# Kernel optimization log

Hardware: AMD Instinct MI355X
Metric: run time of the kernel (lower is better)

## Reference

```python
import jax, jax.numpy as jnp
import numpy as np

MARGIN = 0.2
BETA = 0.8333333
EPS = 1e-8          # torch cosine_similarity eps
BIG = 1.0e9         # sentinel used by the torch code for masking

B, M, FEAT, RES = 64, 2048, 512, 32


def setup_inputs() -> dict:
    key = jax.random.key(0)
    k1, k2, k3, k4 = jax.random.split(key, 4)
    return {
        "anchor_features": jax.random.normal(k1, (B, FEAT), dtype=jnp.float32),
        "true_voxels": jax.random.uniform(k2, (B, RES, RES, RES), dtype=jnp.float32),
        "memory_keys": jax.random.normal(k3, (M, FEAT), dtype=jnp.float32),
        "memory_values": jax.random.uniform(k4, (M, RES, RES, RES), dtype=jnp.float32),
    }


def reference(anchor_features, true_voxels, memory_keys, memory_values):
    b = true_voxels.shape[0]
    m = memory_values.shape[0]
    v = true_voxels.reshape(b, -1)        # (B, N) with N = res^3
    w = memory_values.reshape(m, -1)      # (M, N)
    n = v.shape[1]

    # Pairwise voxel MSE via ||a||^2 - 2ab + ||b||^2 GEMM trick (same math,
    # avoids the (B, M, N) broadcast intermediate).
    v_sq = jnp.sum(v * v, axis=1)                         # (B,)
    w_sq = jnp.sum(w * w, axis=1)                         # (M,)
    mse = (v_sq[:, None] + w_sq[None, :] - 2.0 * (v @ w.T)) / n   # (B, M)
    sv_scores = 1.0 - mse

    pos_mask = sv_scores > BETA
    neg_mask = sv_scores < BETA

    # Pairwise cosine distance 1 - cos_sim (norms clamped at eps like torch).
    a_norm = jnp.maximum(jnp.linalg.norm(anchor_features, axis=1, keepdims=True), EPS)
    k_norm = jnp.maximum(jnp.linalg.norm(memory_keys, axis=1, keepdims=True), EPS)
    key_dists = 1.0 - (anchor_features / a_norm) @ (memory_keys / k_norm).T  # (B, M)

    hardest_pos = jnp.max(jnp.where(pos_mask, key_dists, -BIG), axis=1)  # (B,)
    hardest_neg = jnp.min(jnp.where(neg_mask, key_dists, BIG), axis=1)   # (B,)

    loss = jnp.maximum(hardest_pos - hardest_neg + MARGIN, 0.0)          # (B,)

    valid = jnp.any(pos_mask, axis=1) & jnp.any(neg_mask, axis=1)        # (B,)
    cnt = jnp.sum(valid.astype(loss.dtype))
    total = jnp.sum(jnp.where(valid, loss, 0.0))
    # Masked mean; 0.0 when no valid triplets (mirrors the torch early-return).
    return jnp.where(cnt > 0, total / jnp.maximum(cnt, 1.0), 0.0)
```

## Files before the change

### kernel.cpp

```cpp
#include <hip/hip_runtime.h>


typedef __attribute__((ext_vector_type(8)))  short bf16x8;
typedef __attribute__((ext_vector_type(16))) float f32x16;

constexpr int   Mdim   = 2048;
constexpr int   Nvox   = 32768;
constexpr int   NS     = 32;
constexpr float BETA   = 0.8333333f;
constexpr float MARGIN = 0.2f;
constexpr float BIGV   = 1.0e9f;

constexpr size_t OFF_VSQ  = 0;
constexpr size_t OFF_AINV = 64;
constexpr size_t OFF_KINV = 128;
constexpr size_t OFF_WSQ  = 2176;
constexpr size_t OFF_WSQP = 4224;
constexpr size_t OFF_PHP  = 69760;
constexpr size_t OFF_PHN  = 70016;
constexpr size_t OFF_PAP  = 70272;
constexpr size_t OFF_PAN  = 70528;
constexpr size_t OFF_KEYP = 70784;
constexpr size_t OFF_DOTP = 201856;
constexpr size_t OFF_VHI  = 4396160;
constexpr size_t OFF_VLO  = 5444736;

__device__ __forceinline__ unsigned int bf16rne(float x) {
    unsigned int u = __float_as_uint(x);
    return (u + 0x7FFFu + ((u >> 16) & 1u)) >> 16;
}
__device__ __forceinline__ int pk2(unsigned int lo, unsigned int hi) {
    return (int)(lo | (hi << 16));
}
__device__ __forceinline__ void async16(const ushort* g, ushort* l) {
    __builtin_amdgcn_global_load_lds(
        (const __attribute__((address_space(1))) unsigned int*)g,
        (__attribute__((address_space(3))) unsigned int*)l, 16, 0, 0);
}

__global__ __launch_bounds__(256) void prep_kernel(
    const float* __restrict__ vox, const float* __restrict__ anc,
    const float* __restrict__ keys,
    ushort* __restrict__ vhi, ushort* __restrict__ vlo,
    float* __restrict__ vsq, float* __restrict__ ainv, float* __restrict__ kinv)
{
    const int tid = threadIdx.x;
    const int lane = tid & 63;
    const int wave = tid >> 6;
    if (blockIdx.x < 512) {
        #pragma unroll
        for (int u = 0; u < 2; ++u) {
            const int uid = blockIdx.x * 8 + wave * 2 + u;
            const int bh = uid & 1, s = (uid >> 1) & 3, c = uid >> 3;
            const int b   = bh * 32 + (lane & 31);
            const int col = c * 64 + s * 16 + (lane >> 5) * 8;
            const float4* src = reinterpret_cast<const float4*>(vox + (size_t)b * Nvox + col);
            const float4 x0 = src[0], x1 = src[1];
            const float e[8] = {x0.x, x0.y, x0.z, x0.w, x1.x, x1.y, x1.z, x1.w};
            unsigned int h[8], l8[8];
            #pragma unroll
            for (int q = 0; q < 8; ++q) {
                const unsigned int hb = bf16rne(e[q]);
                h[q] = hb;
                l8[q] = bf16rne(e[q] - __uint_as_float(hb << 16));
            }
            const int4 hp = { pk2(h[0],h[1]), pk2(h[2],h[3]), pk2(h[4],h[5]), pk2(h[6],h[7]) };
            const int4 lp = { pk2(l8[0],l8[1]), pk2(l8[2],l8[3]), pk2(l8[4],l8[5]), pk2(l8[6],l8[7]) };
            const size_t base = (size_t)c * 4096 + bh * 2048 + s * 512 + lane * 8;
            *reinterpret_cast<int4*>(vhi + base) = hp;
            *reinterpret_cast<int4*>(vlo + base) = lp;
        }
    } else if (blockIdx.x < 576) {
        const int b = blockIdx.x - 512;
        const float4* src = reinterpret_cast<const float4*>(vox + (size_t)b * Nvox);
        float p = 0.f;
        for (int i = tid; i < Nvox / 4; i += 256) {
            const float4 x = src[i];
            p = fmaf(x.x, x.x, p); p = fmaf(x.y, x.y, p);
            p = fmaf(x.z, x.z, p); p = fmaf(x.w, x.w, p);
        }
        #pragma unroll
        for (int off = 32; off > 0; off >>= 1) p += __shfl_down(p, off);
        __shared__ float sb[4];
        if (lane == 0) sb[wave] = p;
        __syncthreads();
        if (tid == 0) vsq[b] = sb[0] + sb[1] + sb[2] + sb[3];
    } else {
        const int r = (blockIdx.x - 576) * 4 + wave;
        const float* src = (r < 64) ? (anc + (size_t)r * 512)
                                    : (keys + (size_t)(r - 64) * 512);
        const float4* s4 = reinterpret_cast<const float4*>(src);
        const float4 x = s4[lane];
        const float4 y = s4[lane + 64];
        float p = 0.f;
        p = fmaf(x.x, x.x, p); p = fmaf(x.y, x.y, p);
        p = fmaf(x.z, x.z, p); p = fmaf(x.w, x.w, p);
        p = fmaf(y.x, y.x, p); p = fmaf(y.y, y.y, p);
        p = fmaf(y.z, y.z, p); p = fmaf(y.w, y.w, p);
        #pragma unroll
        for (int off = 32; off > 0; off >>= 1) p += __shfl_down(p, off);
        if (lane == 0) {
            const float inv = 1.f / fmaxf(sqrtf(p), 1e-8f);
            if (r < 64) ainv[r] = inv; else kinv[r - 64] = inv;
        }
    }
}

__global__ __launch_bounds__(256, 4) void gemm_big(
    const ushort* __restrict__ vhi, const ushort* __restrict__ vlo,
    const float* __restrict__ W,
    float* __restrict__ dotp, float* __restrict__ wsqp)
{
    __shared__ ushort sVhi[4096], sVlo[4096], sW[4096];
    __shared__ float red[256];

    const int tid  = threadIdx.x;
    const int lane = tid & 63;
    const int wave = tid >> 6;
    const int mb   = blockIdx.x & 31;
    const int ns   = blockIdx.x >> 5;
    const int srow = tid >> 2;
    const int sq   = tid & 3;

    const float*  wptr = W + (size_t)(mb * 64 + srow) * Nvox + ns * 1024 + sq * 4;
    const ushort* vhig = vhi + (size_t)(ns * 16) * 4096 + wave * 1024 + lane * 8;
    const ushort* vlog = vlo + (size_t)(ns * 16) * 4096 + wave * 1024 + lane * 8;
    ushort* ldsVhi = &sVhi[wave * 1024];
    ushort* ldsVlo = &sVlo[wave * 1024];

    const int wr = wave >> 1, wc = wave & 1;
    f32x16 acc = {};
    float wsq = 0.f;

    float4 wreg[4];
    #pragma unroll
    for (int j = 0; j < 4; ++j) wreg[j] = *reinterpret_cast<const float4*>(wptr + j * 16);

    const int woffbase = (srow >> 5) * 2048 + ((srow & 31) + 32 * (sq >> 1)) * 8 + (sq & 1) * 4;

    for (int ch = 0; ch < 16; ++ch) {
        int2 pj[4];
        #pragma unroll
        for (int j = 0; j < 4; ++j) {
            const float e[4] = {wreg[j].x, wreg[j].y, wreg[j].z, wreg[j].w};
            unsigned int hb[4];
            #pragma unroll
            for (int q = 0; q < 4; ++q) {
                wsq = fmaf(e[q], e[q], wsq);
                hb[q] = bf16rne(e[q]);
            }
            pj[j] = (int2){ pk2(hb[0], hb[1]), pk2(hb[2], hb[3]) };
        }
        __syncthreads();
        async16(vhig + (size_t)ch * 4096,       ldsVhi);
        async16(vhig + (size_t)ch * 4096 + 512, ldsVhi + 512);
        async16(vlog + (size_t)ch * 4096,       ldsVlo);
        async16(vlog + (size_t)ch * 4096 + 512, ldsVlo + 512);
        #pragma unroll
        for (int j = 0; j < 4; ++j)
            *reinterpret_cast<int2*>(&sW[woffbase + j * 512]) = pj[j];
        if (ch < 15) {
            #pragma unroll
            for (int j = 0; j < 4; ++j)
                wreg[j] = *reinterpret_cast<const float4*>(wptr + (ch + 1) * 64 + j * 16);
        }
        __syncthreads();
        #pragma unroll
        for (int s = 0; s < 4; ++s) {
            const bf16x8 ah = *reinterpret_cast<const bf16x8*>(&sVhi[wr * 2048 + s * 512 + lane * 8]);
            const bf16x8 al = *reinterpret_cast<const bf16x8*>(&sVlo[wr * 2048 + s * 512 + lane * 8]);
            const bf16x8 bh = *reinterpret_cast<const bf16x8*>(&sW[wc * 2048 + s * 512 + lane * 8]);
            acc = __builtin_amdgcn_mfma_f32_32x32x16_bf16(ah, bh, acc, 0, 0, 0);
            acc = __builtin_amdgcn_mfma_f32_32x32x16_bf16(al, bh, acc, 0, 0, 0);
        }
    }

    const int col   = lane & 31;
    const int rbase = 4 * (lane >> 5);
    const size_t out_m = (size_t)(mb * 64 + wc * 32 + col);
    #pragma unroll
    for (int r = 0; r < 16; ++r) {
        const int row = (r & 3) + 8 * (r >> 2) + rbase;
        const int b   = wr * 32 + row;
        dotp[(size_t)(ns * 64 + b) * Mdim + out_m] = acc[r];
    }
    red[tid] = wsq;
    __syncthreads();
    if (tid < 64)
        wsqp[(size_t)ns * Mdim + mb * 64 + tid] =
            red[tid*4] + red[tid*4+1] + red[tid*4+2] + red[tid*4+3];
}

__global__ __launch_bounds__(256) void keydist_kernel(
    const float* __restrict__ anc, const float* __restrict__ keys,
    const float* __restrict__ wsqp, float* __restrict__ keyp,
    float* __restrict__ wsq)
{
    const int tid = threadIdx.x;
    if (blockIdx.x >= 256) {
        const int m = (blockIdx.x - 256) * 256 + tid;
        float s = 0.f;
        #pragma unroll
        for (int sp = 0; sp < NS; ++sp) s += wsqp[(size_t)sp * Mdim + m];
        wsq[m] = s;
        return;
    }
    __shared__ float kk[8 * 516];
    const int mt = blockIdx.x * 8;
    {
        const int row = tid >> 5, colb = (tid & 31) * 16;
        const float4* src = reinterpret_cast<const float4*>(keys + (size_t)(mt + row) * 512 + colb);
        #pragma unroll
        for (int j = 0; j < 4; ++j)
            *reinterpret_cast<float4*>(&kk[row * 516 + colb + j * 4]) = src[j];
    }
    __syncthreads();
    const int b = tid >> 2, msub = tid & 3;
    const float* arow = anc + (size_t)b * 512;
    const float* k0 = &kk[msub * 516];
    const float* k1 = &kk[(msub + 4) * 516];
    float d0 = 0.f, d1 = 0.f;
    for (int k = 0; k < 512; k += 4) {
        const float4 a = *reinterpret_cast<const float4*>(arow + k);
        const float4 x = *reinterpret_cast<const float4*>(k0 + k);
        const float4 y = *reinterpret_cast<const float4*>(k1 + k);
        d0 = fmaf(a.x, x.x, d0); d0 = fmaf(a.y, x.y, d0);
        d0 = fmaf(a.z, x.z, d0); d0 = fmaf(a.w, x.w, d0);
        d1 = fmaf(a.x, y.x, d1); d1 = fmaf(a.y, y.y, d1);
        d1 = fmaf(a.z, y.z, d1); d1 = fmaf(a.w, y.w, d1);
    }
    keyp[(size_t)b * Mdim + mt + msub]     = d0;
    keyp[(size_t)b * Mdim + mt + msub + 4] = d1;
}

__global__ __launch_bounds__(256) void rowpart_kernel(
    const float* __restrict__ dotp, const float* __restrict__ wsq,
    const float* __restrict__ keyp, const float* __restrict__ vsq,
    const float* __restrict__ ainv, const float* __restrict__ kinv,
    float* __restrict__ php, float* __restrict__ phn,
    float* __restrict__ pap, float* __restrict__ pan)
{
    const int bid = blockIdx.x, tid = threadIdx.x;
    const int b = bid >> 2, sl = bid & 3;
    const float vs = vsq[b];
    const float ai = ainv[b];
    float hp = -BIGV, hn = BIGV, ap = 0.f, an = 0.f;
    #pragma unroll
    for (int rep = 0; rep < 2; ++rep) {
        const int m = sl * 512 + rep * 256 + tid;
        float dot = 0.f;
        #pragma unroll
        for (int s = 0; s < NS; ++s) dot += dotp[(size_t)(s * 64 + b) * Mdim + m];
        const float sv = 1.f - (vs + wsq[m] - 2.f * dot) * (1.f / 32768.f);
        const float kd = 1.f - keyp[(size_t)b * Mdim + m] * ai * kinv[m];
        if (sv > BETA) { ap = 1.f; hp = fmaxf(hp, kd); }
        if (sv < BETA) { an = 1.f; hn = fminf(hn, kd); }
    }
    #pragma unroll
    for (int off = 32; off > 0; off >>= 1) {
        hp = fmaxf(hp, __shfl_down(hp, off));
        hn = fminf(hn, __shfl_down(hn, off));
        ap = fmaxf(ap, __shfl_down(ap, off));
        an = fmaxf(an, __shfl_down(an, off));
    }
    __shared__ float sb[16];
    const int wv = tid >> 6;
    if ((tid & 63) == 0) {
        sb[wv * 4 + 0] = hp; sb[wv * 4 + 1] = hn;
        sb[wv * 4 + 2] = ap; sb[wv * 4 + 3] = an;
    }
    __syncthreads();
    if (tid == 0) {
        for (int w2 = 1; w2 < 4; ++w2) {
            hp = fmaxf(hp, sb[w2 * 4 + 0]);
            hn = fminf(hn, sb[w2 * 4 + 1]);
            ap = fmaxf(ap, sb[w2 * 4 + 2]);
            an = fmaxf(an, sb[w2 * 4 + 3]);
        }
        php[bid] = hp; phn[bid] = hn; pap[bid] = ap; pan[bid] = an;
    }
}

__global__ void final_kernel(const float* __restrict__ php, const float* __restrict__ phn,
                             const float* __restrict__ pap, const float* __restrict__ pan,
                             float* __restrict__ out)
{
    const int t = threadIdx.x;
    float hp = php[t], hn = phn[t], ap = pap[t], an = pan[t];
    hp = fmaxf(hp, __shfl_down(hp, 2)); hp = fmaxf(hp, __shfl_down(hp, 1));
    hn = fminf(hn, __shfl_down(hn, 2)); hn = fminf(hn, __shfl_down(hn, 1));
    ap = fmaxf(ap, __shfl_down(ap, 2)); ap = fmaxf(ap, __shfl_down(ap, 1));
    an = fmaxf(an, __shfl_down(an, 2)); an = fmaxf(an, __shfl_down(an, 1));
    __shared__ float sl[64], sc[64];
    if ((t & 3) == 0) {
        const int b = t >> 2;
        const float valid = (ap > 0.f && an > 0.f) ? 1.f : 0.f;
        sl[b] = fmaxf(hp - hn + MARGIN, 0.f) * valid;
        sc[b] = valid;
    }
    __syncthreads();
    if (t < 64) {
        float l = sl[t], c = sc[t];
        #pragma unroll
        for (int off = 32; off > 0; off >>= 1) {
            l += __shfl_down(l, off);
            c += __shfl_down(c, off);
        }
        if (t == 0) out[0] = (c > 0.f) ? (l / c) : 0.f;
    }
}

extern "C" void kernel_launch(void* const* d_in, const int* in_sizes, int n_in,
                              void* d_out, int out_size, void* d_ws, size_t ws_size,
                              hipStream_t stream) {
    const float* anchor = (const float*)d_in[0];
    const float* voxels = (const float*)d_in[1];
    const float* keys   = (const float*)d_in[2];
    const float* vals   = (const float*)d_in[3];

    float* ws = (float*)d_ws;
    float*  vsq  = ws + OFF_VSQ;
    float*  ainv = ws + OFF_AINV;
    float*  kinv = ws + OFF_KINV;
    float*  wsq  = ws + OFF_WSQ;
    float*  wsqp = ws + OFF_WSQP;
    float*  php  = ws + OFF_PHP;
    float*  phn  = ws + OFF_PHN;
    float*  pap  = ws + OFF_PAP;
    float*  pan  = ws + OFF_PAN;
    float*  keyp = ws + OFF_KEYP;
    float*  dotp = ws + OFF_DOTP;
    ushort* vhi  = (ushort*)(ws + OFF_VHI);
    ushort* vlo  = (ushort*)(ws + OFF_VLO);

    prep_kernel<<<1104, 256, 0, stream>>>(voxels, anchor, keys, vhi, vlo, vsq, ainv, kinv);
    gemm_big<<<32 * NS, 256, 0, stream>>>(vhi, vlo, vals, dotp, wsqp);
    keydist_kernel<<<264, 256, 0, stream>>>(anchor, keys, wsqp, keyp, wsq);
    rowpart_kernel<<<256, 256, 0, stream>>>(dotp, wsq, keyp, vsq, ainv, kinv,
                                            php, phn, pap, pan);
    final_kernel<<<1, 256, 0, stream>>>(php, phn, pap, pan, (float*)d_out);
}
```

Before: 423.7 us.

## Pre-convert memory values to bf16 in prep kernel and stream via async LDS loads

Moves the fp32-to-bf16 conversion and squared-norm accumulation of memory_values out of the GEMM into a separate prep pass that writes a tiled bf16 copy to workspace. The GEMM then loads all three operands with async global-to-LDS copies and raises its occupancy hint. This removes conversion ALU work and register staging from the GEMM's inner loop. The cost is an extra 128 MB write and read of the bf16 buffer through HBM.

```diff
diff --git a/kernel.cpp b/kernel.cpp
--- a/kernel.cpp
+++ b/kernel.cpp
@@ -10,6 +10,7 @@
 constexpr float BETA   = 0.8333333f;
 constexpr float MARGIN = 0.2f;
 constexpr float BIGV   = 1.0e9f;
+constexpr int   WP     = 68;
 
 constexpr size_t OFF_VSQ  = 0;
 constexpr size_t OFF_AINV = 64;
@@ -24,6 +25,7 @@
 constexpr size_t OFF_DOTP = 201856;
 constexpr size_t OFF_VHI  = 4396160;
 constexpr size_t OFF_VLO  = 5444736;
+constexpr size_t OFF_WBF  = 6493312;
 
 __device__ __forceinline__ unsigned int bf16rne(float x) {
     unsigned int u = __float_as_uint(x);
@@ -38,19 +40,72 @@
         (__attribute__((address_space(3))) unsigned int*)l, 16, 0, 0);
 }
 
-__global__ __launch_bounds__(256) void prep_kernel(
+
+__global__ __launch_bounds__(256) void prep_conv(
     const float* __restrict__ vox, const float* __restrict__ anc,
-    const float* __restrict__ keys,
-    ushort* __restrict__ vhi, ushort* __restrict__ vlo,
-    float* __restrict__ vsq, float* __restrict__ ainv, float* __restrict__ kinv)
-{
-    const int tid = threadIdx.x;
+    const float* __restrict__ keys, const float* __restrict__ W,
+    ushort* __restrict__ vhi, ushort* __restrict__ vlo, ushort* __restrict__ wbf,
+    float* __restrict__ vsq, float* __restrict__ ainv, float* __restrict__ kinv,
+    float* __restrict__ wsqp)
+{
+    const int tid  = threadIdx.x;
     const int lane = tid & 63;
     const int wave = tid >> 6;
-    if (blockIdx.x < 512) {
+    __shared__ float lds[64 * WP + 512];
+
+    if (blockIdx.x < 1024) {
+        const int mb = blockIdx.x >> 5, sl = blockIdx.x & 31;
+        const int r = tid >> 2, q = tid & 3;
+        const float* wsrc = W + (size_t)(mb * 64 + r) * Nvox + sl * 1024;
+        ushort* wdst = wbf + (size_t)(mb * 512 + sl * 16) * 4096;
+        const int s_ = tid >> 6, kh = (tid >> 5) & 1, ml = tid & 31;
+        const int rb0 = ml * WP + s_ * 16 + kh * 8;
+        const int rb1 = (32 + ml) * WP + s_ * 16 + kh * 8;
+        float wsqA = 0.f, wsqB = 0.f;
+        for (int c = 0; c < 16; ++c) {
+            const float4 a0 = *reinterpret_cast<const float4*>(wsrc + c * 64      + q * 4);
+            const float4 a1 = *reinterpret_cast<const float4*>(wsrc + c * 64 + 16 + q * 4);
+            const float4 a2 = *reinterpret_cast<const float4*>(wsrc + c * 64 + 32 + q * 4);
+            const float4 a3 = *reinterpret_cast<const float4*>(wsrc + c * 64 + 48 + q * 4);
+            __syncthreads();
+            *reinterpret_cast<float4*>(&lds[r * WP      + q * 4]) = a0;
+            *reinterpret_cast<float4*>(&lds[r * WP + 16 + q * 4]) = a1;
+            *reinterpret_cast<float4*>(&lds[r * WP + 32 + q * 4]) = a2;
+            *reinterpret_cast<float4*>(&lds[r * WP + 48 + q * 4]) = a3;
+            __syncthreads();
+            #pragma unroll
+            for (int u = 0; u < 2; ++u) {
+                const int rb = u ? rb1 : rb0;
+                const float4 f0 = *reinterpret_cast<const float4*>(&lds[rb]);
+                const float4 f1 = *reinterpret_cast<const float4*>(&lds[rb + 4]);
+                const float e[8] = {f0.x, f0.y, f0.z, f0.w, f1.x, f1.y, f1.z, f1.w};
+                unsigned int h[8];
+                float wq = 0.f;
+                #pragma unroll
+                for (int i = 0; i < 8; ++i) {
+                    wq = fmaf(e[i], e[i], wq);
+                    h[i] = bf16rne(e[i]);
+                }
+                if (u) wsqB += wq; else wsqA += wq;
+                const int4 pk = { pk2(h[0],h[1]), pk2(h[2],h[3]),
+                                  pk2(h[4],h[5]), pk2(h[6],h[7]) };
+                *reinterpret_cast<int4*>(wdst + (size_t)c * 4096 + (u * 256 + tid) * 8) = pk;
+            }
+        }
+        __syncthreads();
+        lds[64 * WP + ml * 8 + s_ * 2 + kh]        = wsqA;
+        lds[64 * WP + (32 + ml) * 8 + s_ * 2 + kh] = wsqB;
+        __syncthreads();
+        if (tid < 64) {
+            float s = 0.f;
+            #pragma unroll
+            for (int i = 0; i < 8; ++i) s += lds[64 * WP + tid * 8 + i];
+            wsqp[(size_t)sl * Mdim + mb * 64 + tid] = s;
+        }
+    } else if (blockIdx.x < 1536) {
         #pragma unroll
         for (int u = 0; u < 2; ++u) {
-            const int uid = blockIdx.x * 8 + wave * 2 + u;
+            const int uid = (blockIdx.x - 1024) * 8 + wave * 2 + u;
             const int bh = uid & 1, s = (uid >> 1) & 3, c = uid >> 3;
             const int b   = bh * 32 + (lane & 31);
             const int col = c * 64 + s * 16 + (lane >> 5) * 8;
@@ -70,8 +125,8 @@
             *reinterpret_cast<int4*>(vhi + base) = hp;
             *reinterpret_cast<int4*>(vlo + base) = lp;
         }
-    } else if (blockIdx.x < 576) {
-        const int b = blockIdx.x - 512;
+    } else if (blockIdx.x < 1600) {
+        const int b = blockIdx.x - 1536;
         const float4* src = reinterpret_cast<const float4*>(vox + (size_t)b * Nvox);
         float p = 0.f;
         for (int i = tid; i < Nvox / 4; i += 256) {
@@ -81,12 +136,11 @@
         }
         #pragma unroll
         for (int off = 32; off > 0; off >>= 1) p += __shfl_down(p, off);
-        __shared__ float sb[4];
-        if (lane == 0) sb[wave] = p;
-        __syncthreads();
-        if (tid == 0) vsq[b] = sb[0] + sb[1] + sb[2] + sb[3];
+        if (lane == 0) lds[wave] = p;
+        __syncthreads();
+        if (tid == 0) vsq[b] = lds[0] + lds[1] + lds[2] + lds[3];
     } else {
-        const int r = (blockIdx.x - 576) * 4 + wave;
+        const int r = (blockIdx.x - 1600) * 4 + wave;
         const float* src = (r < 64) ? (anc + (size_t)r * 512)
                                     : (keys + (size_t)(r - 64) * 512);
         const float4* s4 = reinterpret_cast<const float4*>(src);
@@ -106,64 +160,36 @@
     }
 }
 
-__global__ __launch_bounds__(256, 4) void gemm_big(
+__global__ __launch_bounds__(256, 6) void gemm2(
     const ushort* __restrict__ vhi, const ushort* __restrict__ vlo,
-    const float* __restrict__ W,
-    float* __restrict__ dotp, float* __restrict__ wsqp)
+    const ushort* __restrict__ wbf, float* __restrict__ dotp)
 {
     __shared__ ushort sVhi[4096], sVlo[4096], sW[4096];
-    __shared__ float red[256];
 
     const int tid  = threadIdx.x;
     const int lane = tid & 63;
     const int wave = tid >> 6;
     const int mb   = blockIdx.x & 31;
     const int ns   = blockIdx.x >> 5;
-    const int srow = tid >> 2;
-    const int sq   = tid & 3;
-
-    const float*  wptr = W + (size_t)(mb * 64 + srow) * Nvox + ns * 1024 + sq * 4;
+
     const ushort* vhig = vhi + (size_t)(ns * 16) * 4096 + wave * 1024 + lane * 8;
     const ushort* vlog = vlo + (size_t)(ns * 16) * 4096 + wave * 1024 + lane * 8;
-    ushort* ldsVhi = &sVhi[wave * 1024];
-    ushort* ldsVlo = &sVlo[wave * 1024];
+    const ushort* wg   = wbf + (size_t)(mb * 512 + ns * 16) * 4096 + wave * 1024 + lane * 8;
+    ushort* dVhi = &sVhi[wave * 1024];
+    ushort* dVlo = &sVlo[wave * 1024];
+    ushort* dW   = &sW[wave * 1024];
 
     const int wr = wave >> 1, wc = wave & 1;
     f32x16 acc = {};
-    float wsq = 0.f;
-
-    float4 wreg[4];
-    #pragma unroll
-    for (int j = 0; j < 4; ++j) wreg[j] = *reinterpret_cast<const float4*>(wptr + j * 16);
-
-    const int woffbase = (srow >> 5) * 2048 + ((srow & 31) + 32 * (sq >> 1)) * 8 + (sq & 1) * 4;
 
     for (int ch = 0; ch < 16; ++ch) {
-        int2 pj[4];
-        #pragma unroll
-        for (int j = 0; j < 4; ++j) {
-            const float e[4] = {wreg[j].x, wreg[j].y, wreg[j].z, wreg[j].w};
-            unsigned int hb[4];
-            #pragma unroll
-            for (int q = 0; q < 4; ++q) {
-                wsq = fmaf(e[q], e[q], wsq);
-                hb[q] = bf16rne(e[q]);
-            }
-            pj[j] = (int2){ pk2(hb[0], hb[1]), pk2(hb[2], hb[3]) };
-        }
-        __syncthreads();
-        async16(vhig + (size_t)ch * 4096,       ldsVhi);
-        async16(vhig + (size_t)ch * 4096 + 512, ldsVhi + 512);
-        async16(vlog + (size_t)ch * 4096,       ldsVlo);
-        async16(vlog + (size_t)ch * 4096 + 512, ldsVlo + 512);
-        #pragma unroll
-        for (int j = 0; j < 4; ++j)
-            *reinterpret_cast<int2*>(&sW[woffbase + j * 512]) = pj[j];
-        if (ch < 15) {
-            #pragma unroll
-            for (int j = 0; j < 4; ++j)
-                wreg[j] = *reinterpret_cast<const float4*>(wptr + (ch + 1) * 64 + j * 16);
-        }
+        __syncthreads();
+        async16(vhig + (size_t)ch * 4096,       dVhi);
+        async16(vhig + (size_t)ch * 4096 + 512, dVhi + 512);
+        async16(vlog + (size_t)ch * 4096,       dVlo);
+        async16(vlog + (size_t)ch * 4096 + 512, dVlo + 512);
+        async16(wg   + (size_t)ch * 4096,       dW);
+        async16(wg   + (size_t)ch * 4096 + 512, dW + 512);
         __syncthreads();
         #pragma unroll
         for (int s = 0; s < 4; ++s) {
@@ -184,11 +210,6 @@
         const int b   = wr * 32 + row;
         dotp[(size_t)(ns * 64 + b) * Mdim + out_m] = acc[r];
     }
-    red[tid] = wsq;
-    __syncthreads();
-    if (tid < 64)
-        wsqp[(size_t)ns * Mdim + mb * 64 + tid] =
-            red[tid*4] + red[tid*4+1] + red[tid*4+2] + red[tid*4+3];
 }
 
 __global__ __launch_bounds__(256) void keydist_kernel(
@@ -332,9 +353,11 @@
     float*  dotp = ws + OFF_DOTP;
     ushort* vhi  = (ushort*)(ws + OFF_VHI);
     ushort* vlo  = (ushort*)(ws + OFF_VLO);
-
-    prep_kernel<<<1104, 256, 0, stream>>>(voxels, anchor, keys, vhi, vlo, vsq, ainv, kinv);
-    gemm_big<<<32 * NS, 256, 0, stream>>>(vhi, vlo, vals, dotp, wsqp);
+    ushort* wbf  = (ushort*)(ws + OFF_WBF);
+
+    prep_conv<<<2128, 256, 0, stream>>>(voxels, anchor, keys, vals,
+                                        vhi, vlo, wbf, vsq, ainv, kinv, wsqp);
+    gemm2<<<32 * NS, 256, 0, stream>>>(vhi, vlo, wbf, dotp);
     keydist_kernel<<<264, 256, 0, stream>>>(anchor, keys, wsqp, keyp, wsq);
     rowpart_kernel<<<256, 256, 0, stream>>>(dotp, wsq, keyp, vsq, ainv, kinv,
                                             php, phn, pap, pan);
```

Result: slower. 477.3 us (+12.6%).

## Restructure voxel GEMM to keep voxel slab in LDS and stream W in registers

Applied to the files above, without the earlier changes.

The GEMM now loads a 64-batch hi/lo bf16 voxel slab of 256 columns into a 64KB LDS buffer per phase. Each wave converts its own 32 memory rows of W straight from global into MFMA A-fragments in registers, so the W-to-LDS staging and the per-chunk double barrier go away. Each block covers 128 M rows with two accumulators, and the launch drops to 512 blocks at occupancy 2. The dot-product partials and key-distance outputs are transposed to an (m, b) layout, and the row and final reductions are rewritten so that lanes map to batch. The risks are lower occupancy from the large LDS footprint and uncoalesced per-lane W row loads.

```diff
diff --git a/kernel.cpp b/kernel.cpp
--- a/kernel.cpp
+++ b/kernel.cpp
@@ -17,13 +17,12 @@
 constexpr size_t OFF_WSQ  = 2176;
 constexpr size_t OFF_WSQP = 4224;
 constexpr size_t OFF_PHP  = 69760;
-constexpr size_t OFF_PHN  = 70016;
-constexpr size_t OFF_PAP  = 70272;
-constexpr size_t OFF_PAN  = 70528;
-constexpr size_t OFF_KEYP = 70784;
-constexpr size_t OFF_DOTP = 201856;
-constexpr size_t OFF_VHI  = 4396160;
-constexpr size_t OFF_VLO  = 5444736;
+constexpr size_t OFF_PHN  = 86144;
+constexpr size_t OFF_PAP  = 102528;
+constexpr size_t OFF_PAN  = 118912;
+constexpr size_t OFF_KEYPT= 135296;
+constexpr size_t OFF_DOTP = 266368;
+constexpr size_t OFF_VF   = 4460672;
 
 __device__ __forceinline__ unsigned int bf16rne(float x) {
     unsigned int u = __float_as_uint(x);
@@ -38,23 +37,24 @@
         (__attribute__((address_space(3))) unsigned int*)l, 16, 0, 0);
 }
 
+
 __global__ __launch_bounds__(256) void prep_kernel(
     const float* __restrict__ vox, const float* __restrict__ anc,
-    const float* __restrict__ keys,
-    ushort* __restrict__ vhi, ushort* __restrict__ vlo,
+    const float* __restrict__ keys, ushort* __restrict__ vf,
     float* __restrict__ vsq, float* __restrict__ ainv, float* __restrict__ kinv)
 {
     const int tid = threadIdx.x;
     const int lane = tid & 63;
     const int wave = tid >> 6;
-    if (blockIdx.x < 512) {
-        #pragma unroll
-        for (int u = 0; u < 2; ++u) {
-            const int uid = blockIdx.x * 8 + wave * 2 + u;
-            const int bh = uid & 1, s = (uid >> 1) & 3, c = uid >> 3;
-            const int b   = bh * 32 + (lane & 31);
-            const int col = c * 64 + s * 16 + (lane >> 5) * 8;
-            const float4* src = reinterpret_cast<const float4*>(vox + (size_t)b * Nvox + col);
+    __shared__ float sb[4];
+
+    if (blockIdx.x < 256) {
+        #pragma unroll
+        for (int it = 0; it < 4; ++it) {
+            const int g = blockIdx.x * 16 + wave * 4 + it;
+            const int k0 = g * 8;
+            const int slice = g >> 5, gg = g & 31;
+            const float4* src = reinterpret_cast<const float4*>(vox + (size_t)lane * Nvox + k0);
             const float4 x0 = src[0], x1 = src[1];
             const float e[8] = {x0.x, x0.y, x0.z, x0.w, x1.x, x1.y, x1.z, x1.w};
             unsigned int h[8], l8[8];
@@ -66,12 +66,12 @@
             }
             const int4 hp = { pk2(h[0],h[1]), pk2(h[2],h[3]), pk2(h[4],h[5]), pk2(h[6],h[7]) };
             const int4 lp = { pk2(l8[0],l8[1]), pk2(l8[2],l8[3]), pk2(l8[4],l8[5]), pk2(l8[6],l8[7]) };
-            const size_t base = (size_t)c * 4096 + bh * 2048 + s * 512 + lane * 8;
-            *reinterpret_cast<int4*>(vhi + base) = hp;
-            *reinterpret_cast<int4*>(vlo + base) = lp;
-        }
-    } else if (blockIdx.x < 576) {
-        const int b = blockIdx.x - 512;
+            const size_t base = (size_t)slice * 32768 + gg * 512 + lane * 8;
+            *reinterpret_cast<int4*>(vf + base)         = hp;
+            *reinterpret_cast<int4*>(vf + base + 16384) = lp;
+        }
+    } else if (blockIdx.x < 320) {
+        const int b = blockIdx.x - 256;
         const float4* src = reinterpret_cast<const float4*>(vox + (size_t)b * Nvox);
         float p = 0.f;
         for (int i = tid; i < Nvox / 4; i += 256) {
@@ -81,12 +81,11 @@
         }
         #pragma unroll
         for (int off = 32; off > 0; off >>= 1) p += __shfl_down(p, off);
-        __shared__ float sb[4];
         if (lane == 0) sb[wave] = p;
         __syncthreads();
         if (tid == 0) vsq[b] = sb[0] + sb[1] + sb[2] + sb[3];
     } else {
-        const int r = (blockIdx.x - 576) * 4 + wave;
+        const int r = (blockIdx.x - 320) * 4 + wave;
         const float* src = (r < 64) ? (anc + (size_t)r * 512)
                                     : (keys + (size_t)(r - 64) * 512);
         const float4* s4 = reinterpret_cast<const float4*>(src);
@@ -106,94 +105,81 @@
     }
 }
 
-__global__ __launch_bounds__(256, 4) void gemm_big(
-    const ushort* __restrict__ vhi, const ushort* __restrict__ vlo,
-    const float* __restrict__ W,
+__global__ __launch_bounds__(256, 2) void gemm3(
+    const ushort* __restrict__ vf, const float* __restrict__ W,
     float* __restrict__ dotp, float* __restrict__ wsqp)
 {
-    __shared__ ushort sVhi[4096], sVlo[4096], sW[4096];
-    __shared__ float red[256];
+    __shared__ ushort sV[32768];
 
     const int tid  = threadIdx.x;
     const int lane = tid & 63;
     const int wave = tid >> 6;
-    const int mb   = blockIdx.x & 31;
-    const int ns   = blockIdx.x >> 5;
-    const int srow = tid >> 2;
-    const int sq   = tid & 3;
-
-    const float*  wptr = W + (size_t)(mb * 64 + srow) * Nvox + ns * 1024 + sq * 4;
-    const ushort* vhig = vhi + (size_t)(ns * 16) * 4096 + wave * 1024 + lane * 8;
-    const ushort* vlog = vlo + (size_t)(ns * 16) * 4096 + wave * 1024 + lane * 8;
-    ushort* ldsVhi = &sVhi[wave * 1024];
-    ushort* ldsVlo = &sVlo[wave * 1024];
-
-    const int wr = wave >> 1, wc = wave & 1;
-    f32x16 acc = {};
+    const int mb   = blockIdx.x & 15;
+    const int ns   = blockIdx.x >> 4;
+
+    const int   mrow = mb * 128 + wave * 32 + (lane & 31);
+    const float* wrow = W + (size_t)mrow * Nvox + ns * 1024 + (lane >> 5) * 8;
+
+    f32x16 acc0 = {}, acc1 = {};
     float wsq = 0.f;
 
-    float4 wreg[4];
-    #pragma unroll
-    for (int j = 0; j < 4; ++j) wreg[j] = *reinterpret_cast<const float4*>(wptr + j * 16);
-
-    const int woffbase = (srow >> 5) * 2048 + ((srow & 31) + 32 * (sq >> 1)) * 8 + (sq & 1) * 4;
-
-    for (int ch = 0; ch < 16; ++ch) {
-        int2 pj[4];
-        #pragma unroll
-        for (int j = 0; j < 4; ++j) {
-            const float e[4] = {wreg[j].x, wreg[j].y, wreg[j].z, wreg[j].w};
-            unsigned int hb[4];
+    for (int p = 0; p < 4; ++p) {
+        if (p) __syncthreads();
+        const ushort* vg = vf + (size_t)(ns * 4 + p) * 32768 + wave * 512 + lane * 8;
+        ushort* vl = &sV[wave * 512];
+        #pragma unroll
+        for (int r = 0; r < 16; ++r)
+            async16(vg + r * 2048, vl + r * 2048);
+        __syncthreads();
+
+        const float* wp = wrow + p * 256;
+        float4 wa = *reinterpret_cast<const float4*>(wp);
+        float4 wb = *reinterpret_cast<const float4*>(wp + 4);
+        #pragma unroll 4
+        for (int ch = 0; ch < 16; ++ch) {
+            const float e[8] = {wa.x, wa.y, wa.z, wa.w, wb.x, wb.y, wb.z, wb.w};
+            unsigned int h[8];
             #pragma unroll
-            for (int q = 0; q < 4; ++q) {
+            for (int q = 0; q < 8; ++q) {
                 wsq = fmaf(e[q], e[q], wsq);
-                hb[q] = bf16rne(e[q]);
+                h[q] = bf16rne(e[q]);
             }
-            pj[j] = (int2){ pk2(hb[0], hb[1]), pk2(hb[2], hb[3]) };
-        }
-        __syncthreads();
-        async16(vhig + (size_t)ch * 4096,       ldsVhi);
-        async16(vhig + (size_t)ch * 4096 + 512, ldsVhi + 512);
-        async16(vlog + (size_t)ch * 4096,       ldsVlo);
-        async16(vlog + (size_t)ch * 4096 + 512, ldsVlo + 512);
-        #pragma unroll
-        for (int j = 0; j < 4; ++j)
-            *reinterpret_cast<int2*>(&sW[woffbase + j * 512]) = pj[j];
-        if (ch < 15) {
-            #pragma unroll
-            for (int j = 0; j < 4; ++j)
-                wreg[j] = *reinterpret_cast<const float4*>(wptr + (ch + 1) * 64 + j * 16);
-        }
-        __syncthreads();
-        #pragma unroll
-        for (int s = 0; s < 4; ++s) {
-            const bf16x8 ah = *reinterpret_cast<const bf16x8*>(&sVhi[wr * 2048 + s * 512 + lane * 8]);
-            const bf16x8 al = *reinterpret_cast<const bf16x8*>(&sVlo[wr * 2048 + s * 512 + lane * 8]);
-            const bf16x8 bh = *reinterpret_cast<const bf16x8*>(&sW[wc * 2048 + s * 512 + lane * 8]);
-            acc = __builtin_amdgcn_mfma_f32_32x32x16_bf16(ah, bh, acc, 0, 0, 0);
-            acc = __builtin_amdgcn_mfma_f32_32x32x16_bf16(al, bh, acc, 0, 0, 0);
-        }
-    }
-
-    const int col   = lane & 31;
-    const int rbase = 4 * (lane >> 5);
-    const size_t out_m = (size_t)(mb * 64 + wc * 32 + col);
+            int4 pk = { pk2(h[0],h[1]), pk2(h[2],h[3]), pk2(h[4],h[5]), pk2(h[6],h[7]) };
+            const bf16x8 af = *reinterpret_cast<const bf16x8*>(&pk);
+            if (ch < 15) {
+                wa = *reinterpret_cast<const float4*>(wp + (ch + 1) * 16);
+                wb = *reinterpret_cast<const float4*>(wp + (ch + 1) * 16 + 4);
+            }
+            const int ro = (ch * 2 + (lane >> 5)) * 512 + (lane & 31) * 8;
+            const bf16x8 bh0 = *reinterpret_cast<const bf16x8*>(&sV[ro]);
+            const bf16x8 bh1 = *reinterpret_cast<const bf16x8*>(&sV[ro + 256]);
+            const bf16x8 bl0 = *reinterpret_cast<const bf16x8*>(&sV[16384 + ro]);
+            const bf16x8 bl1 = *reinterpret_cast<const bf16x8*>(&sV[16384 + ro + 256]);
+            acc0 = __builtin_amdgcn_mfma_f32_32x32x16_bf16(af, bh0, acc0, 0, 0, 0);
+            acc0 = __builtin_amdgcn_mfma_f32_32x32x16_bf16(af, bl0, acc0, 0, 0, 0);
+            acc1 = __builtin_amdgcn_mfma_f32_32x32x16_bf16(af, bh1, acc1, 0, 0, 0);
+            acc1 = __builtin_amdgcn_mfma_f32_32x32x16_bf16(af, bl1, acc1, 0, 0, 0);
+        }
+    }
+
+    wsq += __shfl_down(wsq, 32);
+    if (lane < 32)
+        wsqp[(size_t)ns * Mdim + mb * 128 + wave * 32 + lane] = wsq;
+
+    const int bcol = lane & 31;
+    const int rb   = 4 * (lane >> 5);
     #pragma unroll
     for (int r = 0; r < 16; ++r) {
-        const int row = (r & 3) + 8 * (r >> 2) + rbase;
-        const int b   = wr * 32 + row;
-        dotp[(size_t)(ns * 64 + b) * Mdim + out_m] = acc[r];
-    }
-    red[tid] = wsq;
-    __syncthreads();
-    if (tid < 64)
-        wsqp[(size_t)ns * Mdim + mb * 64 + tid] =
-            red[tid*4] + red[tid*4+1] + red[tid*4+2] + red[tid*4+3];
+        const int m = mb * 128 + wave * 32 + (r & 3) + 8 * (r >> 2) + rb;
+        float* dst = dotp + ((size_t)ns * Mdim + m) * 64;
+        dst[bcol]      = acc0[r];
+        dst[32 + bcol] = acc1[r];
+    }
 }
 
 __global__ __launch_bounds__(256) void keydist_kernel(
     const float* __restrict__ anc, const float* __restrict__ keys,
-    const float* __restrict__ wsqp, float* __restrict__ keyp,
+    const float* __restrict__ wsqp, float* __restrict__ keypt,
     float* __restrict__ wsq)
 {
     const int tid = threadIdx.x;
@@ -215,10 +201,10 @@
             *reinterpret_cast<float4*>(&kk[row * 516 + colb + j * 4]) = src[j];
     }
     __syncthreads();
-    const int b = tid >> 2, msub = tid & 3;
+    const int b = tid & 63, mi = tid >> 6;
     const float* arow = anc + (size_t)b * 512;
-    const float* k0 = &kk[msub * 516];
-    const float* k1 = &kk[(msub + 4) * 516];
+    const float* k0 = &kk[mi * 516];
+    const float* k1 = &kk[(mi + 4) * 516];
     float d0 = 0.f, d1 = 0.f;
     for (int k = 0; k < 512; k += 4) {
         const float4 a = *reinterpret_cast<const float4*>(arow + k);
@@ -229,55 +215,52 @@
         d1 = fmaf(a.x, y.x, d1); d1 = fmaf(a.y, y.y, d1);
         d1 = fmaf(a.z, y.z, d1); d1 = fmaf(a.w, y.w, d1);
     }
-    keyp[(size_t)b * Mdim + mt + msub]     = d0;
-    keyp[(size_t)b * Mdim + mt + msub + 4] = d1;
+    keypt[(size_t)(mt + mi) * 64 + b]     = d0;
+    keypt[(size_t)(mt + 4 + mi) * 64 + b] = d1;
 }
 
 __global__ __launch_bounds__(256) void rowpart_kernel(
     const float* __restrict__ dotp, const float* __restrict__ wsq,
-    const float* __restrict__ keyp, const float* __restrict__ vsq,
+    const float* __restrict__ keypt, const float* __restrict__ vsq,
     const float* __restrict__ ainv, const float* __restrict__ kinv,
     float* __restrict__ php, float* __restrict__ phn,
     float* __restrict__ pap, float* __restrict__ pan)
 {
-    const int bid = blockIdx.x, tid = threadIdx.x;
-    const int b = bid >> 2, sl = bid & 3;
-    const float vs = vsq[b];
-    const float ai = ainv[b];
+    const int tid = threadIdx.x, lane = tid & 63, wave = tid >> 6;
+    const int mbase = blockIdx.x * 8;
+    const float vs = vsq[lane];
+    const float ai = ainv[lane];
     float hp = -BIGV, hn = BIGV, ap = 0.f, an = 0.f;
     #pragma unroll
-    for (int rep = 0; rep < 2; ++rep) {
-        const int m = sl * 512 + rep * 256 + tid;
+    for (int it = 0; it < 2; ++it) {
+        const int m = mbase + it * 4 + wave;
         float dot = 0.f;
         #pragma unroll
-        for (int s = 0; s < NS; ++s) dot += dotp[(size_t)(s * 64 + b) * Mdim + m];
+        for (int s = 0; s < NS; ++s)
+            dot += dotp[((size_t)s * Mdim + m) * 64 + lane];
         const float sv = 1.f - (vs + wsq[m] - 2.f * dot) * (1.f / 32768.f);
-        const float kd = 1.f - keyp[(size_t)b * Mdim + m] * ai * kinv[m];
+        const float kd = 1.f - keypt[(size_t)m * 64 + lane] * ai * kinv[m];
         if (sv > BETA) { ap = 1.f; hp = fmaxf(hp, kd); }
         if (sv < BETA) { an = 1.f; hn = fminf(hn, kd); }
     }
-    #pragma unroll
-    for (int off = 32; off > 0; off >>= 1) {
-        hp = fmaxf(hp, __shfl_down(hp, off));
-        hn = fminf(hn, __shfl_down(hn, off));
-        ap = fmaxf(ap, __shfl_down(ap, off));
-        an = fmaxf(an, __shfl_down(an, off));
-    }
-    __shared__ float sb[16];
-    const int wv = tid >> 6;
-    if ((tid & 63) == 0) {
-        sb[wv * 4 + 0] = hp; sb[wv * 4 + 1] = hn;
-        sb[wv * 4 + 2] = ap; sb[wv * 4 + 3] = an;
-    }
+    __shared__ float red[4 * 64 * 4];
+    red[(wave * 64 + lane) * 4 + 0] = hp;
+    red[(wave * 64 + lane) * 4 + 1] = hn;
+    red[(wave * 64 + lane) * 4 + 2] = ap;
+    red[(wave * 64 + lane) * 4 + 3] = an;
     __syncthreads();
-    if (tid == 0) {
-        for (int w2 = 1; w2 < 4; ++w2) {
-            hp = fmaxf(hp, sb[w2 * 4 + 0]);
-            hn = fminf(hn, sb[w2 * 4 + 1]);
-            ap = fmaxf(ap, sb[w2 * 4 + 2]);
-            an = fmaxf(an, sb[w2 * 4 + 3]);
-        }
-        php[bid] = hp; phn[bid] = hn; pap[bid] = ap; pan[bid] = an;
+    if (tid < 64) {
+        #pragma unroll
+        for (int w = 1; w < 4; ++w) {
+            hp = fmaxf(hp, red[(w * 64 + tid) * 4 + 0]);
+            hn = fminf(hn, red[(w * 64 + tid) * 4 + 1]);
+            ap = fmaxf(ap, red[(w * 64 + tid) * 4 + 2]);
+            an = fmaxf(an, red[(w * 64 + tid) * 4 + 3]);
+        }
+        php[blockIdx.x * 64 + tid] = hp;
+        phn[blockIdx.x * 64 + tid] = hn;
+        pap[blockIdx.x * 64 + tid] = ap;
+        pan[blockIdx.x * 64 + tid] = an;
     }
 }
 
@@ -286,21 +269,28 @@
                              float* __restrict__ out)
 {
     const int t = threadIdx.x;
-    float hp = php[t], hn = phn[t], ap = pap[t], an = pan[t];
-    hp = fmaxf(hp, __shfl_down(hp, 2)); hp = fmaxf(hp, __shfl_down(hp, 1));
-    hn = fminf(hn, __shfl_down(hn, 2)); hn = fminf(hn, __shfl_down(hn, 1));
-    ap = fmaxf(ap, __shfl_down(ap, 2)); ap = fmaxf(ap, __shfl_down(ap, 1));
-    an = fmaxf(an, __shfl_down(an, 2)); an = fmaxf(an, __shfl_down(an, 1));
-    __shared__ float sl[64], sc[64];
-    if ((t & 3) == 0) {
-        const int b = t >> 2;
-        const float valid = (ap > 0.f && an > 0.f) ? 1.f : 0.f;
-        sl[b] = fmaxf(hp - hn + MARGIN, 0.f) * valid;
-        sc[b] = valid;
-    }
+    const int b = t & 63, q = t >> 6;
+    float hp = -BIGV, hn = BIGV, ap = 0.f, an = 0.f;
+    for (int g = q; g < 256; g += 4) {
+        hp = fmaxf(hp, php[g * 64 + b]);
+        hn = fminf(hn, phn[g * 64 + b]);
+        ap = fmaxf(ap, pap[g * 64 + b]);
+        an = fmaxf(an, pan[g * 64 + b]);
+    }
+    __shared__ float R[256 * 4];
+    R[t * 4 + 0] = hp; R[t * 4 + 1] = hn; R[t * 4 + 2] = ap; R[t * 4 + 3] = an;
     __syncthreads();
     if (t < 64) {
-        float l = sl[t], c = sc[t];
+        #pragma unroll
+        for (int q2 = 1; q2 < 4; ++q2) {
+            hp = fmaxf(hp, R[((q2 << 6) + t) * 4 + 0]);
+            hn = fminf(hn, R[((q2 << 6) + t) * 4 + 1]);
+            ap = fmaxf(ap, R[((q2 << 6) + t) * 4 + 2]);
+            an = fmaxf(an, R[((q2 << 6) + t) * 4 + 3]);
+        }
+        const float valid = (ap > 0.f && an > 0.f) ? 1.f : 0.f;
+        float l = fmaxf(hp - hn + MARGIN, 0.f) * valid;
+        float c = valid;
         #pragma unroll
         for (int off = 32; off > 0; off >>= 1) {
             l += __shfl_down(l, off);
@@ -319,24 +309,23 @@
     const float* vals   = (const float*)d_in[3];
 
     float* ws = (float*)d_ws;
-    float*  vsq  = ws + OFF_VSQ;
-    float*  ainv = ws + OFF_AINV;
-    float*  kinv = ws + OFF_KINV;
-    float*  wsq  = ws + OFF_WSQ;
-    float*  wsqp = ws + OFF_WSQP;
-    float*  php  = ws + OFF_PHP;
-    float*  phn  = ws + OFF_PHN;
-    float*  pap  = ws + OFF_PAP;
-    float*  pan  = ws + OFF_PAN;
-    float*  keyp = ws + OFF_KEYP;
-    float*  dotp = ws + OFF_DOTP;
-    ushort* vhi  = (ushort*)(ws + OFF_VHI);
-    ushort* vlo  = (ushort*)(ws + OFF_VLO);
-
-    prep_kernel<<<1104, 256, 0, stream>>>(voxels, anchor, keys, vhi, vlo, vsq, ainv, kinv);
-    gemm_big<<<32 * NS, 256, 0, stream>>>(vhi, vlo, vals, dotp, wsqp);
-    keydist_kernel<<<264, 256, 0, stream>>>(anchor, keys, wsqp, keyp, wsq);
-    rowpart_kernel<<<256, 256, 0, stream>>>(dotp, wsq, keyp, vsq, ainv, kinv,
+    float*  vsq   = ws + OFF_VSQ;
+    float*  ainv  = ws + OFF_AINV;
+    float*  kinv  = ws + OFF_KINV;
+    float*  wsq   = ws + OFF_WSQ;
+    float*  wsqp  = ws + OFF_WSQP;
+    float*  php   = ws + OFF_PHP;
+    float*  phn   = ws + OFF_PHN;
+    float*  pap   = ws + OFF_PAP;
+    float*  pan   = ws + OFF_PAN;
+    float*  keypt = ws + OFF_KEYPT;
+    float*  dotp  = ws + OFF_DOTP;
+    ushort* vf    = (ushort*)(ws + OFF_VF);
+
+    prep_kernel<<<848, 256, 0, stream>>>(voxels, anchor, keys, vf, vsq, ainv, kinv);
+    gemm3<<<512, 256, 0, stream>>>(vf, vals, dotp, wsqp);
+    keydist_kernel<<<264, 256, 0, stream>>>(anchor, keys, wsqp, keypt, wsq);
+    rowpart_kernel<<<256, 256, 0, stream>>>(dotp, wsq, keypt, vsq, ainv, kinv,
                                             php, phn, pap, pan);
     final_kernel<<<1, 256, 0, stream>>>(php, phn, pap, pan, (float*)d_out);
 }
```

Measured after the change: 458.1 us. 1.08x slower.
